# Performance work log

Measured on AMD Instinct MI355X. Metric: run time of the kernel, lower is better.

The kernel has to match this reference:

```python
import jax, jax.numpy as jnp
import numpy as np

D_MODEL = 2048
EXPAND = 2
D_INNER = EXPAND * D_MODEL          # 4096 == d_ssm
D_STATE = 128
NGROUPS = 1
HEADDIM = 64
NHEADS = D_INNER // HEADDIM          # 64
D_CONV = 4
CHUNK = 128
D_XBC = D_INNER + 2 * NGROUPS * D_STATE   # 4352
D_IN_PROJ = 2 * D_INNER + 2 * NGROUPS * D_STATE + NHEADS  # 8512
EPS = 1e-5


def setup_inputs() -> dict:
    key = jax.random.key(0)
    ks = jax.random.split(key, 9)
    u = jax.random.normal(ks[0], (2, 2048, D_MODEL), dtype=jnp.float32)
    W_in = jax.random.normal(ks[1], (D_IN_PROJ, D_MODEL), dtype=jnp.float32) / np.sqrt(D_MODEL)
    conv_w = jax.random.normal(ks[2], (D_XBC, D_CONV), dtype=jnp.float32) / np.sqrt(D_CONV)
    conv_b = jax.random.normal(ks[3], (D_XBC,), dtype=jnp.float32) * 0.1
    dt_bias = jnp.log(jnp.expm1(jax.random.uniform(ks[4], (NHEADS,), minval=0.001, maxval=0.1)))
    A_log = jnp.log(jax.random.uniform(ks[5], (NHEADS,), minval=1.0, maxval=16.0))
    D = jnp.ones((NHEADS,), dtype=jnp.float32)
    norm_weight = jnp.ones((D_INNER,), dtype=jnp.float32)
    W_out = jax.random.normal(ks[8], (D_MODEL, D_INNER), dtype=jnp.float32) / np.sqrt(D_INNER)
    return {"u": u, "W_in": W_in, "conv_w": conv_w, "conv_b": conv_b,
            "dt_bias": dt_bias, "A_log": A_log, "D": D,
            "norm_weight": norm_weight, "W_out": W_out}


def _causal_conv1d(xBC, conv_w, conv_b):
    # xBC: [b, l, d]; depthwise causal conv of width D_CONV, then SiLU
    x = jnp.transpose(xBC, (0, 2, 1))                      # [b, d, l]
    x = jnp.pad(x, ((0, 0), (0, 0), (D_CONV - 1, 0)))
    y = jax.lax.conv_general_dilated(
        x, conv_w[:, None, :], window_strides=(1,), padding='VALID',
        feature_group_count=D_XBC, dimension_numbers=('NCH', 'OIH', 'NCH'))
    y = y + conv_b[None, :, None]
    return jnp.transpose(jax.nn.silu(y), (0, 2, 1))        # [b, l, d]


def _ssd(x, dt, A, B, C, D):
    # x: [b,l,h,p]; dt: [b,l,h] (post-softplus); A: [h]; B,C: [b,l,g,n]; D: [h]
    b, L, h, p = x.shape
    n = B.shape[-1]
    c = L // CHUNK
    hpg = h // NGROUPS
    Bh = jnp.repeat(B, hpg, axis=2)                        # [b,l,h,n]
    Ch = jnp.repeat(C, hpg, axis=2)
    xr = x.reshape(b, c, CHUNK, h, p)
    dtr = dt.reshape(b, c, CHUNK, h)
    Br = Bh.reshape(b, c, CHUNK, h, n)
    Cr = Ch.reshape(b, c, CHUNK, h, n)
    xdt = xr * dtr[..., None]                              # [b,c,l,h,p]
    dA = jnp.transpose((dt * A[None, None, :]).reshape(b, c, CHUNK, h), (0, 3, 1, 2))  # [b,h,c,l]
    A_cs = jnp.cumsum(dA, axis=-1)                         # [b,h,c,l]
    # intra-chunk decay matrix L[i,j] = exp(sum_{j+1..i} dA), lower-triangular
    diff = A_cs[..., :, None] - A_cs[..., None, :]         # [b,h,c,l,s]
    mask = jnp.tril(jnp.ones((CHUNK, CHUNK), dtype=bool))
    Lmat = jnp.where(mask, jnp.exp(jnp.where(mask, diff, 0.0)), 0.0)
    Y_diag = jnp.einsum('bclhn,bcshn,bhcls,bcshp->bclhp', Cr, Br, Lmat, xdt)
    decay_states = jnp.exp(A_cs[..., -1:] - A_cs)          # [b,h,c,l]
    states = jnp.einsum('bclhn,bhcl,bclhp->bchpn', Br, decay_states, xdt)
    chunk_decay = jnp.exp(A_cs[..., -1])                   # [b,h,c]
    # inter-chunk recurrence over c chunks
    def step(carry, inp):
        s, d = inp                                         # s:[b,h,p,n], d:[b,h]
        return carry * d[..., None, None] + s, carry
    init = jnp.zeros((b, h, p, n), dtype=x.dtype)
    _, prev = jax.lax.scan(step, init,
                           (jnp.transpose(states, (1, 0, 2, 3, 4)),
                            jnp.transpose(chunk_decay, (2, 0, 1))))
    prev_states = jnp.transpose(prev, (1, 0, 2, 3, 4))     # [b,c,h,p,n]
    Y_off = jnp.einsum('bclhn,bchpn,bhcl->bclhp', Cr, prev_states, jnp.exp(A_cs))
    Y = (Y_diag + Y_off).reshape(b, L, h, p) + x * D[None, None, :, None]
    return Y


def reference(u, W_in, conv_w, conv_b, dt_bias, A_log, D, norm_weight, W_out):
    b, L, _ = u.shape
    zxbcdt = jnp.einsum('bld,ed->ble', u, W_in)            # [b,l,8512]
    z = zxbcdt[..., :D_INNER]
    xBC = zxbcdt[..., D_INNER:D_INNER + D_XBC]
    dt = zxbcdt[..., D_INNER + D_XBC:]                     # [b,l,h]
    xBC = _causal_conv1d(xBC, conv_w, conv_b)
    x = xBC[..., :D_INNER]
    B = xBC[..., D_INNER:D_INNER + NGROUPS * D_STATE].reshape(b, L, NGROUPS, D_STATE)
    C = xBC[..., D_INNER + NGROUPS * D_STATE:].reshape(b, L, NGROUPS, D_STATE)
    dt = jax.nn.softplus(dt + dt_bias[None, None, :])
    A = -jnp.exp(A_log)
    y = _ssd(x.reshape(b, L, NHEADS, HEADDIM), dt, A, B, C, D)
    y = y.reshape(b, L, D_INNER)
    # gated RMSNorm (norm_before_gate=False): norm(y * silu(z))
    yg = y * jax.nn.silu(z)
    y = yg * jax.lax.rsqrt(jnp.mean(yg * yg, axis=-1, keepdims=True) + EPS) * norm_weight
    return jnp.einsum('bld,ed->ble', y, W_out)
```

## Files before the change

### kernel.cpp

```cpp
#include <hip/hip_runtime.h>
#include <cstdint>
#include <cstddef>

#define SEQ     2048
#define NBATCH  2
#define BL      (NBATCH*SEQ)
#define DMODEL  2048
#define DINNER  4096
#define DSTATE  128
#define HEADDIM 64
#define NHEADS  64
#define DXBC    4352
#define DPROJ   8512
#define NPAD    8704
#define NCHUNK  16
#define CHUNKL  128

typedef __bf16 bf16x8_t __attribute__((ext_vector_type(8)));
typedef float f32x4_t __attribute__((ext_vector_type(4)));
typedef unsigned short u16x8_t __attribute__((ext_vector_type(8)));
typedef unsigned short u16x4_t __attribute__((ext_vector_type(4)));
typedef __attribute__((address_space(1))) unsigned int as1_u32;
typedef __attribute__((address_space(3))) unsigned int as3_u32;

__device__ __forceinline__ unsigned short f2bf(float f) {
  unsigned u = __builtin_bit_cast(unsigned, f);
  u += 0x7FFFu + ((u >> 16) & 1u);
  return (unsigned short)(u >> 16);
}
__device__ __forceinline__ float bf2f(unsigned short h) {
  unsigned u = ((unsigned)h) << 16;
  return __builtin_bit_cast(float, u);
}
__device__ __forceinline__ void gload16(const void* g, void* l) {
  __builtin_amdgcn_global_load_lds((const as1_u32*)g, (as3_u32*)l, 16, 0, 0);
}
__device__ __forceinline__ f32x4_t mfma16(u16x8_t a, u16x8_t b, f32x4_t c) {
  return __builtin_amdgcn_mfma_f32_16x16x32_bf16(
      __builtin_bit_cast(bf16x8_t, a), __builtin_bit_cast(bf16x8_t, b), c, 0, 0, 0);
}
__device__ __forceinline__ float siluf(float x) { return x / (1.f + __expf(-x)); }

__global__ __launch_bounds__(256) void cvt_kernel(const float* __restrict__ src,
                                                  unsigned short* __restrict__ dst, int n) {
  int idx = (blockIdx.x * 256 + threadIdx.x) * 4;
  if (idx >= n) return;
  float4 v = *(const float4*)&src[idx];
  u16x4_t o; o[0] = f2bf(v.x); o[1] = f2bf(v.y); o[2] = f2bf(v.z); o[3] = f2bf(v.w);
  *(u16x4_t*)&dst[idx] = o;
}

__global__ __launch_bounds__(256) void cvt_win_kernel(const float* __restrict__ W,
                                                      unsigned short* __restrict__ dst) {
  int idx = (blockIdx.x * 256 + threadIdx.x) * 4;
  if (idx >= NPAD * DMODEL) return;
  int e = idx / DMODEL;
  u16x4_t o;
  if (e < DPROJ) {
    float4 v = *(const float4*)&W[idx];
    o[0] = f2bf(v.x); o[1] = f2bf(v.y); o[2] = f2bf(v.z); o[3] = f2bf(v.w);
  } else {
    o[0] = 0; o[1] = 0; o[2] = 0; o[3] = 0;
  }
  *(u16x4_t*)&dst[idx] = o;
}

template <int WM, bool BF16OUT>
__global__ __launch_bounds__(512, 2) void gemm256_kernel(const unsigned short* __restrict__ A,
                                                         const unsigned short* __restrict__ B,
                                                         void* __restrict__ Cp,
                                                         int M, int N, int K, int gx) {
  constexpr int BM  = 32 * WM;
  constexpr int AUB = BM * 64;
  constexpr int BUB = 16384;
  constexpr int BUF = AUB + BUB;
  constexpr int LA  = AUB / 8192;
  constexpr int LB  = 2;
  __shared__ __attribute__((aligned(16))) char lds[4 * BUF];

  const int nwg = gridDim.x;
  const int q8 = nwg >> 3;
  const int lid = blockIdx.x;
  const int newid = (lid & 7) * q8 + (lid >> 3);
  const int band = newid / (gx * 4);
  const int idx  = newid % (gx * 4);
  const int n0 = (idx >> 2) * 256;
  const int m0 = (band * 4 + (idx & 3)) * BM;

  const int t = threadIdx.x, lane = t & 63, w = t >> 6;
  const int wm = w >> 2, wn = w & 3;
  const int NK = K >> 5;
  const int kslot = (lane >> 4) * 16;

  f32x4_t acc[WM][4];
#pragma unroll
  for (int i = 0; i < WM; ++i)
#pragma unroll
    for (int j = 0; j < 4; ++j) acc[i][j] = (f32x4_t){0.f, 0.f, 0.f, 0.f};

  auto stage_unit = [&](int u) {
    if (u >= 2 * NK) return;
    const int Tt = u >> 1;
    char* base = lds + (Tt & 3) * BUF + ((u & 1) ? AUB : 0);
    const unsigned short* G = (u & 1) ? B : A;
    const int g0 = (u & 1) ? n0 : m0;
    const int k0 = Tt << 5;
    if (u & 1) {
#pragma unroll
      for (int i = 0; i < LB; ++i) {
        int o = i * 8192 + t * 16;
        int row = o >> 6;
        int cb = (o & 63) ^ (((row >> 1) & 3) << 4);
        gload16(&G[(size_t)(g0 + row) * K + k0 + (cb >> 1)], base + o);
      }
    } else {
#pragma unroll
      for (int i = 0; i < LA; ++i) {
        int o = i * 8192 + t * 16;
        int row = o >> 6;
        int cb = (o & 63) ^ (((row >> 1) & 3) << 4);
        gload16(&G[(size_t)(g0 + row) * K + k0 + (cb >> 1)], base + o);
      }
    }
  };
  auto rdA = [&](int bq, int mr) -> u16x8_t {
    int row = wm * (BM / 2) + mr * 16 + (lane & 15);
    int byte = bq * BUF + row * 64 + (kslot ^ (((row >> 1) & 3) << 4));
    return *(const u16x8_t*)(lds + byte);
  };
  auto rdB = [&](int bq, int nr) -> u16x8_t {
    int row = wn * 64 + nr * 16 + (lane & 15);
    int byte = bq * BUF + AUB + row * 64 + (kslot ^ (((row >> 1) & 3) << 4));
    return *(const u16x8_t*)(lds + byte);
  };

#pragma unroll
  for (int u = 0; u < 6; ++u) stage_unit(u);
  if constexpr (WM == 8) asm volatile("s_waitcnt vmcnt(8)" ::: "memory");
  else                   asm volatile("s_waitcnt vmcnt(6)" ::: "memory");
  asm volatile("" ::: "memory");
  __builtin_amdgcn_s_barrier();

  for (int T = 0; T < NK; ++T) {
    const int bq = T & 3;
    u16x8_t af[WM], bfr[4];
#pragma unroll
    for (int mr = 0; mr < WM; ++mr) af[mr] = rdA(bq, mr);
    bfr[0] = rdB(bq, 0);
    bfr[1] = rdB(bq, 1);
    stage_unit(2 * T + 6);
    asm volatile("" ::: "memory");
    __builtin_amdgcn_s_barrier();
    asm volatile("s_waitcnt lgkmcnt(0)" ::: "memory");
    __builtin_amdgcn_sched_barrier(0);
    __builtin_amdgcn_s_setprio(1);
#pragma unroll
    for (int mr = 0; mr < WM; ++mr) {
      acc[mr][0] = mfma16(af[mr], bfr[0], acc[mr][0]);
      acc[mr][1] = mfma16(af[mr], bfr[1], acc[mr][1]);
    }
    __builtin_amdgcn_s_setprio(0);
    asm volatile("" ::: "memory");
    __builtin_amdgcn_s_barrier();
    bfr[2] = rdB(bq, 2);
    bfr[3] = rdB(bq, 3);
    stage_unit(2 * T + 7);
    asm volatile("s_waitcnt lgkmcnt(0)" ::: "memory");
    __builtin_amdgcn_sched_barrier(0);
    __builtin_amdgcn_s_setprio(1);
#pragma unroll
    for (int mr = 0; mr < WM; ++mr) {
      acc[mr][2] = mfma16(af[mr], bfr[2], acc[mr][2]);
      acc[mr][3] = mfma16(af[mr], bfr[3], acc[mr][3]);
    }
    __builtin_amdgcn_s_setprio(0);
    if (T < NK - 3) {
      if constexpr (WM == 8) asm volatile("s_waitcnt vmcnt(8)" ::: "memory");
      else                   asm volatile("s_waitcnt vmcnt(6)" ::: "memory");
    } else if (T == NK - 3) {
      if constexpr (WM == 8) asm volatile("s_waitcnt vmcnt(4)" ::: "memory");
      else                   asm volatile("s_waitcnt vmcnt(3)" ::: "memory");
    } else if (T == NK - 2) {
      asm volatile("s_waitcnt vmcnt(0)" ::: "memory");
    }
    asm volatile("" ::: "memory");
    __builtin_amdgcn_s_barrier();
  }

#pragma unroll
  for (int mr = 0; mr < WM; ++mr) {
    const int mbase = m0 + wm * (BM / 2) + mr * 16 + (lane >> 4) * 4;
#pragma unroll
    for (int nr = 0; nr < 4; ++nr) {
      const int n = n0 + wn * 64 + nr * 16 + (lane & 15);
#pragma unroll
      for (int r = 0; r < 4; ++r) {
        if (BF16OUT) ((unsigned short*)Cp)[(size_t)(mbase + r) * N + n] = f2bf(acc[mr][nr][r]);
        else         ((float*)Cp)[(size_t)(mbase + r) * N + n] = acc[mr][nr][r];
      }
    }
  }
}

__global__ __launch_bounds__(256) void conv_kernel(const unsigned short* __restrict__ zx,
                                                   const float* __restrict__ conv_w,
                                                   const float* __restrict__ conv_b,
                                                   unsigned short* __restrict__ xc) {
  long long idx = (long long)blockIdx.x * 256 + threadIdx.x;
  if (idx >= (long long)BL * DXBC) return;
  int e = (int)(idx % DXBC);
  int bl = (int)(idx / DXBC);
  int l = bl % SEQ, b = bl / SEQ;
  float acc = conv_b[e];
#pragma unroll
  for (int wi = 0; wi < 4; ++wi) {
    int ll = l - 3 + wi;
    if (ll >= 0) acc += bf2f(zx[((size_t)b * SEQ + ll) * NPAD + DINNER + e]) * conv_w[e * 4 + wi];
  }
  xc[(size_t)bl * DXBC + e] = f2bf(siluf(acc));
}

__global__ __launch_bounds__(128) void dt_kernel(const unsigned short* __restrict__ zx,
                                                 const float* __restrict__ dt_bias,
                                                 const float* __restrict__ A_log,
                                                 float* __restrict__ dt_soft,
                                                 float* __restrict__ Acs,
                                                 float* __restrict__ cdecay) {
  int blk = blockIdx.x;
  int c = blk & 15, h = (blk >> 4) & 63, b = blk >> 10;
  int i = threadIdx.x;
  int l = c * CHUNKL + i;
  float raw = bf2f(zx[((size_t)b * SEQ + l) * NPAD + (DINNER + DXBC) + h]) + dt_bias[h];
  float dt = (raw > 20.f) ? raw : log1pf(__expf(raw));
  dt_soft[((size_t)b * 64 + h) * SEQ + l] = dt;
  float A = -__expf(A_log[h]);
  __shared__ float sbuf[128];
  sbuf[i] = dt * A;
  __syncthreads();
  for (int ofs = 1; ofs < 128; ofs <<= 1) {
    float v = (i >= ofs) ? sbuf[i - ofs] : 0.f;
    __syncthreads();
    sbuf[i] += v;
    __syncthreads();
  }
  float cs = sbuf[i];
  Acs[(((size_t)b * 64 + h) * 16 + c) * 128 + i] = cs;
  if (i == 127) cdecay[((size_t)b * 64 + h) * 16 + c] = __expf(cs);
}

__global__ __launch_bounds__(256) void xdt_kernel(const unsigned short* __restrict__ xc,
                                                  const float* __restrict__ dt_soft,
                                                  unsigned short* __restrict__ xdtT) {
  int blk = blockIdx.x;
  int lt = blk & 15, h = (blk >> 4) & 63, b = blk >> 10;
  __shared__ unsigned short tile[128][66];
  __shared__ float dts[128];
  int t = threadIdx.x;
  const unsigned short* xg = xc + ((size_t)b * SEQ + lt * 128) * DXBC + h * 64;
#pragma unroll
  for (int k = 0; k < 32; ++k) {
    int idx = t + k * 256;
    int row = idx >> 6, col = idx & 63;
    tile[row][col] = xg[(size_t)row * DXBC + col];
  }
  if (t < 128) dts[t] = dt_soft[((size_t)b * 64 + h) * SEQ + lt * 128 + t];
  __syncthreads();
  unsigned short* xo = xdtT + (((size_t)b * 64 + h) * 64) * SEQ + lt * 128;
#pragma unroll
  for (int k = 0; k < 32; ++k) {
    int idx = t + k * 256;
    int p = idx >> 7, j = idx & 127;
    xo[(size_t)p * SEQ + j] = f2bf(bf2f(tile[j][p]) * dts[j]);
  }
}

__global__ __launch_bounds__(256) void btr_kernel(const unsigned short* __restrict__ xc,
                                                  unsigned short* __restrict__ BT) {
  int blk = blockIdx.x;
  int lt = blk & 15, b = blk >> 4;
  __shared__ unsigned short tile[128][129];
  int t = threadIdx.x;
  const unsigned short* src = xc + ((size_t)b * SEQ + lt * 128) * DXBC + DINNER;
#pragma unroll
  for (int k = 0; k < 64; ++k) {
    int idx = t + k * 256;
    int j = idx >> 7, n = idx & 127;
    tile[j][n] = src[(size_t)j * DXBC + n];
  }
  __syncthreads();
  unsigned short* dst = BT + (size_t)b * 128 * SEQ + lt * 128;
#pragma unroll
  for (int k = 0; k < 64; ++k) {
    int idx = t + k * 256;
    int n = idx >> 7, j = idx & 127;
    dst[(size_t)n * SEQ + j] = tile[j][n];
  }
}

__global__ __launch_bounds__(256) void ssd_states_kernel(const unsigned short* __restrict__ BT,
                                                         const unsigned short* __restrict__ xdtT,
                                                         const float* __restrict__ Acs,
                                                         float* __restrict__ states) {
  int blk = blockIdx.x;
  int h = blk & 63, c = (blk >> 6) & 15, b = blk >> 10;
  __shared__ unsigned short BTs[128 * 128];
  __shared__ unsigned short xs[64 * 128];
  __shared__ float dec[128];
  int t = threadIdx.x, lane = t & 63, w = t >> 6, wr = w >> 1, wc = w & 1;
  int srow = t >> 4, scol = (t & 15) * 8;
  const unsigned short* BTb = BT + (size_t)b * 128 * SEQ + c * 128;
#pragma unroll
  for (int s = 0; s < 8; ++s) {
    int r = s * 16 + srow;
    gload16(&BTb[(size_t)r * SEQ + scol], &BTs[r * 128 + scol]);
  }
  const unsigned short* xb = xdtT + (((size_t)b * 64 + h) * 64) * SEQ + c * 128;
#pragma unroll
  for (int s = 0; s < 4; ++s) {
    int r = s * 16 + srow;
    gload16(&xb[(size_t)r * SEQ + scol], &xs[r * 128 + scol]);
  }
  const float* acsr = Acs + (((size_t)b * 64 + h) * 16 + c) * 128;
  float alast = acsr[127];
  if (t < 128) dec[t] = __expf(alast - acsr[t]);
  __syncthreads();

  f32x4_t acc[2][4];
#pragma unroll
  for (int i = 0; i < 2; ++i)
#pragma unroll
    for (int j = 0; j < 4; ++j) acc[i][j] = (f32x4_t){0.f, 0.f, 0.f, 0.f};
#pragma unroll
  for (int ks = 0; ks < 4; ++ks) {
    const int kk = ks * 32 + (lane >> 4) * 8;
    float d8[8];
#pragma unroll
    for (int e = 0; e < 8; ++e) d8[e] = dec[kk + e];
    u16x8_t af[2], bfr[4];
#pragma unroll
    for (int i = 0; i < 2; ++i) {
      u16x8_t raw = *(const u16x8_t*)&xs[(wr * 32 + i * 16 + (lane & 15)) * 128 + kk];
      u16x8_t sc;
#pragma unroll
      for (int e = 0; e < 8; ++e) sc[e] = f2bf(bf2f(raw[e]) * d8[e]);
      af[i] = sc;
    }
#pragma unroll
    for (int j = 0; j < 4; ++j)
      bfr[j] = *(const u16x8_t*)&BTs[(wc * 64 + j * 16 + (lane & 15)) * 128 + kk];
#pragma unroll
    for (int i = 0; i < 2; ++i)
#pragma unroll
      for (int j = 0; j < 4; ++j) acc[i][j] = mfma16(af[i], bfr[j], acc[i][j]);
  }
  float* so = states + ((((size_t)b * 16 + c) * 64 + h) * 64) * 128;
#pragma unroll
  for (int i = 0; i < 2; ++i) {
    int pbase = wr * 32 + i * 16 + (lane >> 4) * 4;
#pragma unroll
    for (int j = 0; j < 4; ++j) {
      int n = wc * 64 + j * 16 + (lane & 15);
#pragma unroll
      for (int r = 0; r < 4; ++r) so[(size_t)(pbase + r) * 128 + n] = acc[i][j][r];
    }
  }
}

__global__ __launch_bounds__(256) void ssd_scan_kernel(const float* __restrict__ states,
                                                       const float* __restrict__ cdecay,
                                                       unsigned short* __restrict__ prevb) {
  int blk = blockIdx.x;
  int s = blk & 7, h = (blk >> 3) & 63, b = blk >> 9;
  int t = threadIdx.x;
  float carry[4] = {0.f, 0.f, 0.f, 0.f};
  const float* cd = cdecay + ((size_t)b * 64 + h) * 16;
  for (int c = 0; c < 16; ++c) {
    const float* sp = states + (((size_t)(b * 16 + c) * 64 + h) * 64) * 128;
    unsigned short* pp = prevb + (((size_t)(b * 16 + c) * 64 + h) * 64) * 128;
    float d = cd[c];
#pragma unroll
    for (int k = 0; k < 4; ++k) {
      int e = s * 1024 + k * 256 + t;
      pp[e] = f2bf(carry[k]);
      carry[k] = carry[k] * d + sp[e];
    }
  }
}

__global__ __launch_bounds__(256) void ssd_y_kernel(const unsigned short* __restrict__ xc,
                                                    const unsigned short* __restrict__ xdtT,
                                                    const unsigned short* __restrict__ prevb,
                                                    const float* __restrict__ Acs,
                                                    const float* __restrict__ Dp,
                                                    unsigned short* __restrict__ Y) {
  int blk = blockIdx.x;
  int h = blk & 63, c = (blk >> 6) & 15, b = blk >> 10;
  __shared__ unsigned short Bs[128 * 128];
  __shared__ unsigned short Cs[128 * 128];
  __shared__ unsigned short xs[64 * 128];
  __shared__ unsigned short ps[64 * 128];
  __shared__ float acs_s[128];
  int t = threadIdx.x, lane = t & 63, w = t >> 6, wr = w >> 1, wc = w & 1;
  int srow = t >> 4, scol = (t & 15) * 8;
  const unsigned short* Bg = xc + ((size_t)b * SEQ + c * 128) * DXBC + DINNER;
  const unsigned short* Cg = Bg + DSTATE;
#pragma unroll
  for (int s = 0; s < 8; ++s) {
    int r = s * 16 + srow;
    gload16(&Bg[(size_t)r * DXBC + scol], &Bs[r * 128 + scol]);
    gload16(&Cg[(size_t)r * DXBC + scol], &Cs[r * 128 + scol]);
  }
  const unsigned short* xg = xdtT + (((size_t)b * 64 + h) * 64) * SEQ + c * 128;
#pragma unroll
  for (int s = 0; s < 4; ++s) {
    int r = s * 16 + srow;
    gload16(&xg[(size_t)r * SEQ + scol], &xs[r * 128 + scol]);
  }
  const unsigned short* pg = prevb + ((((size_t)b * 16 + c) * 64 + h) * 64) * 128;
#pragma unroll
  for (int s = 0; s < 4; ++s) {
    int r = s * 16 + srow;
    gload16(&pg[r * 128 + scol], &ps[r * 128 + scol]);
  }
  const float* acsr = Acs + (((size_t)b * 64 + h) * 16 + c) * 128;
  if (t < 128) acs_s[t] = acsr[t];
  __syncthreads();

  f32x4_t cbt[4][4];
#pragma unroll
  for (int i = 0; i < 4; ++i)
#pragma unroll
    for (int j = 0; j < 4; ++j) cbt[i][j] = (f32x4_t){0.f, 0.f, 0.f, 0.f};
#pragma unroll
  for (int ks = 0; ks < 4; ++ks) {
    const int kk = ks * 32 + (lane >> 4) * 8;
    u16x8_t af[4], bfr[4];
#pragma unroll
    for (int i = 0; i < 4; ++i) {
      af[i]  = *(const u16x8_t*)&Bs[(wr * 64 + i * 16 + (lane & 15)) * 128 + kk];
      bfr[i] = *(const u16x8_t*)&Cs[(wc * 64 + i * 16 + (lane & 15)) * 128 + kk];
    }
#pragma unroll
    for (int i = 0; i < 4; ++i)
#pragma unroll
      for (int j = 0; j < 4; ++j) cbt[i][j] = mfma16(af[i], bfr[j], cbt[i][j]);
  }
  __syncthreads();
#pragma unroll
  for (int fi = 0; fi < 4; ++fi) {
#pragma unroll
    for (int fj = 0; fj < 4; ++fj) {
      int i = wc * 64 + fj * 16 + (lane & 15);
      int jb = wr * 64 + fi * 16 + (lane >> 4) * 4;
      float ai = acs_s[i];
      u16x4_t m4;
#pragma unroll
      for (int r = 0; r < 4; ++r) {
        int j = jb + r;
        float v = (i >= j) ? cbt[fi][fj][r] * __expf(ai - acs_s[j]) : 0.f;
        m4[r] = f2bf(v);
      }
      *(u16x4_t*)&Bs[i * 128 + jb] = m4;
    }
  }
  __syncthreads();

  f32x4_t accY[4][2], accO[4][2];
#pragma unroll
  for (int i = 0; i < 4; ++i)
#pragma unroll
    for (int j = 0; j < 2; ++j) {
      accY[i][j] = (f32x4_t){0.f, 0.f, 0.f, 0.f};
      accO[i][j] = (f32x4_t){0.f, 0.f, 0.f, 0.f};
    }
#pragma unroll
  for (int ks = 0; ks < 4; ++ks) {
    const int kk = ks * 32 + (lane >> 4) * 8;
    u16x8_t af[4], bfr[2], cf[4], pf[2];
#pragma unroll
    for (int i = 0; i < 4; ++i) {
      af[i] = *(const u16x8_t*)&Bs[(wr * 64 + i * 16 + (lane & 15)) * 128 + kk];
      cf[i] = *(const u16x8_t*)&Cs[(wr * 64 + i * 16 + (lane & 15)) * 128 + kk];
    }
#pragma unroll
    for (int j = 0; j < 2; ++j) {
      bfr[j] = *(const u16x8_t*)&xs[(wc * 32 + j * 16 + (lane & 15)) * 128 + kk];
      pf[j]  = *(const u16x8_t*)&ps[(wc * 32 + j * 16 + (lane & 15)) * 128 + kk];
    }
#pragma unroll
    for (int i = 0; i < 4; ++i)
#pragma unroll
      for (int j = 0; j < 2; ++j) {
        accY[i][j] = mfma16(af[i], bfr[j], accY[i][j]);
        accO[i][j] = mfma16(cf[i], pf[j], accO[i][j]);
      }
  }
  float Dh = Dp[h];
  unsigned short* Yo = Y + ((size_t)b * SEQ + c * 128) * DINNER + h * 64;
  const unsigned short* xo = xc + ((size_t)b * SEQ + c * 128) * DXBC + h * 64;
#pragma unroll
  for (int fi = 0; fi < 4; ++fi) {
    int ibase = wr * 64 + fi * 16 + (lane >> 4) * 4;
#pragma unroll
    for (int r = 0; r < 4; ++r) {
      int i = ibase + r;
      float esc = __expf(acs_s[i]);
#pragma unroll
      for (int fj = 0; fj < 2; ++fj) {
        int p = wc * 32 + fj * 16 + (lane & 15);
        float v = accY[fi][fj][r] + accO[fi][fj][r] * esc + bf2f(xo[(size_t)i * DXBC + p]) * Dh;
        Yo[(size_t)i * DINNER + p] = f2bf(v);
      }
    }
  }
}

__global__ __launch_bounds__(256) void norm_kernel(const unsigned short* __restrict__ Y,
                                                   const unsigned short* __restrict__ zx,
                                                   const float* __restrict__ nw,
                                                   unsigned short* __restrict__ yn) {
  int bl = blockIdx.x;
  const unsigned short* yr = Y + (size_t)bl * DINNER;
  const unsigned short* zr = zx + (size_t)bl * NPAD;
  int t = threadIdx.x;
  float vals[16];
  float ss = 0.f;
#pragma unroll
  for (int k = 0; k < 16; ++k) {
    int d = t + k * 256;
    float g = bf2f(yr[d]) * siluf(bf2f(zr[d]));
    vals[k] = g;
    ss += g * g;
  }
#pragma unroll
  for (int o = 32; o > 0; o >>= 1) ss += __shfl_down(ss, o, 64);
  __shared__ float red[4];
  if ((t & 63) == 0) red[t >> 6] = ss;
  __syncthreads();
  float tot = red[0] + red[1] + red[2] + red[3];
  float rs = rsqrtf(tot * (1.f / (float)DINNER) + 1e-5f);
#pragma unroll
  for (int k = 0; k < 16; ++k) {
    int d = t + k * 256;
    yn[(size_t)bl * DINNER + d] = f2bf(vals[k] * rs * nw[d]);
  }
}

extern "C" void kernel_launch(void* const* d_in, const int* in_sizes, int n_in,
                              void* d_out, int out_size, void* d_ws, size_t ws_size,
                              hipStream_t stream) {
  const float* u       = (const float*)d_in[0];
  const float* W_in    = (const float*)d_in[1];
  const float* conv_w  = (const float*)d_in[2];
  const float* conv_b  = (const float*)d_in[3];
  const float* dt_bias = (const float*)d_in[4];
  const float* A_log   = (const float*)d_in[5];
  const float* Dv      = (const float*)d_in[6];
  const float* norm_w  = (const float*)d_in[7];
  const float* W_out   = (const float*)d_in[8];
  float* out = (float*)d_out;
  (void)in_sizes; (void)n_in; (void)out_size;

  const size_t SZ_UBF    = (size_t)BL * DMODEL * 2;
  const size_t SZ_WIN    = (size_t)NPAD * DMODEL * 2;
  const size_t SZ_XDTT   = (size_t)NBATCH * NHEADS * HEADDIM * SEQ * 2;
  const size_t SZ_ZX     = (size_t)BL * NPAD * 2;
  const size_t SZ_XC     = (size_t)BL * DXBC * 2;
  const size_t SZ_BT     = (size_t)NBATCH * DSTATE * SEQ * 2;
  const size_t SZ_DTS    = (size_t)NBATCH * NHEADS * SEQ * 4;
  const size_t SZ_ACS    = (size_t)NBATCH * NHEADS * NCHUNK * 128 * 4;
  const size_t SZ_CDEC   = (size_t)NBATCH * NHEADS * NCHUNK * 4;
  const size_t SZ_STATES = (size_t)NBATCH * NCHUNK * NHEADS * HEADDIM * DSTATE * 4;
  const size_t SZ_PREV   = (size_t)NBATCH * NCHUNK * NHEADS * HEADDIM * DSTATE * 2;
  const size_t REGION_A  = SZ_UBF + SZ_WIN;

  char* ws = (char*)d_ws;
  size_t off = 0;
  auto alloc = [&](size_t bytes) { char* p = ws + off; off += (bytes + 255) & ~(size_t)255; return p; };

  char* regionA = alloc(REGION_A);
  unsigned short* zx     = (unsigned short*)alloc(SZ_ZX);
  unsigned short* xc     = (unsigned short*)alloc(SZ_XC);
  unsigned short* BT     = (unsigned short*)alloc(SZ_BT);
  float* dt_soft         = (float*)alloc(SZ_DTS);
  float* Acs             = (float*)alloc(SZ_ACS);
  float* cdecay          = (float*)alloc(SZ_CDEC);
  char* statesYb         = alloc(SZ_STATES);
  char* prevYn           = alloc(SZ_PREV);
  if (off > ws_size) return;

  unsigned short* u_bf    = (unsigned short*)regionA;
  unsigned short* win_bf  = (unsigned short*)(regionA + SZ_UBF);
  unsigned short* xdtT    = (unsigned short*)regionA;
  unsigned short* wout_bf = (unsigned short*)(regionA + SZ_XDTT);
  float* states           = (float*)statesYb;
  unsigned short* Yb      = (unsigned short*)statesYb;
  unsigned short* prevb   = (unsigned short*)prevYn;
  unsigned short* yn      = (unsigned short*)prevYn;

  cvt_kernel<<<dim3((BL * DMODEL / 4 + 255) / 256), dim3(256), 0, stream>>>(u, u_bf, BL * DMODEL);
  cvt_win_kernel<<<dim3(NPAD * DMODEL / 4 / 256), dim3(256), 0, stream>>>(W_in, win_bf);

  gemm256_kernel<8, true><<<dim3((NPAD / 256) * (BL / 256)), dim3(512), 0, stream>>>(
      u_bf, win_bf, zx, BL, NPAD, DMODEL, NPAD / 256);

  cvt_kernel<<<dim3((DMODEL * DINNER / 4 + 255) / 256), dim3(256), 0, stream>>>(W_out, wout_bf, DMODEL * DINNER);

  conv_kernel<<<dim3((int)(((size_t)BL * DXBC + 255) / 256)), dim3(256), 0, stream>>>(zx, conv_w, conv_b, xc);

  dt_kernel<<<dim3(NBATCH * NHEADS * NCHUNK), dim3(128), 0, stream>>>(zx, dt_bias, A_log, dt_soft, Acs, cdecay);

  xdt_kernel<<<dim3(NBATCH * NHEADS * NCHUNK), dim3(256), 0, stream>>>(xc, dt_soft, xdtT);
  btr_kernel<<<dim3(NBATCH * (SEQ / 128)), dim3(256), 0, stream>>>(xc, BT);

  ssd_states_kernel<<<dim3(NBATCH * NCHUNK * NHEADS), dim3(256), 0, stream>>>(BT, xdtT, Acs, states);
  ssd_scan_kernel<<<dim3(NBATCH * NHEADS * 8), dim3(256), 0, stream>>>(states, cdecay, prevb);
  ssd_y_kernel<<<dim3(NBATCH * NCHUNK * NHEADS), dim3(256), 0, stream>>>(xc, xdtT, prevb, Acs, Dv, Yb);

  norm_kernel<<<dim3(BL), dim3(256), 0, stream>>>(Yb, zx, norm_w, yn);

  gemm256_kernel<4, false><<<dim3((DMODEL / 256) * (BL / 128)), dim3(512), 0, stream>>>(
      yn, wout_bf, out, BL, DMODEL, DINNER, DMODEL / 256);
}
```

Measured before the change: 568.5 us.

## Switch GEMM to double-buffered LDS pipeline and vectorize conv kernel

The GEMM kernel drops from a 4-deep LDS ring with split half-tile MFMA phases to a 2-stage double buffer. Each K step waits on global loads, reads all fragments, issues the next tile's loads and then runs all MFMAs. This halves LDS use, which could raise occupancy, but leaves less prefetch depth to hide global latency. Separately, the depthwise conv kernel now processes 8 channels per thread with 16-byte vector loads and stores instead of one scalar element per thread.

```diff
diff --git a/kernel.cpp b/kernel.cpp
--- a/kernel.cpp
+++ b/kernel.cpp
@@ -76,7 +76,8 @@
   constexpr int BUF = AUB + BUB;
   constexpr int LA  = AUB / 8192;
   constexpr int LB  = 2;
-  __shared__ __attribute__((aligned(16))) char lds[4 * BUF];
+  constexpr int LT  = LA + LB;
+  __shared__ __attribute__((aligned(16))) char lds[2 * BUF];
 
   const int nwg = gridDim.x;
   const int q8 = nwg >> 3;
@@ -101,7 +102,7 @@
   auto stage_unit = [&](int u) {
     if (u >= 2 * NK) return;
     const int Tt = u >> 1;
-    char* base = lds + (Tt & 3) * BUF + ((u & 1) ? AUB : 0);
+    char* base = lds + (Tt & 1) * BUF + ((u & 1) ? AUB : 0);
     const unsigned short* G = (u & 1) ? B : A;
     const int g0 = (u & 1) ? n0 : m0;
     const int k0 = Tt << 5;
@@ -135,56 +136,34 @@
   };
 
 #pragma unroll
-  for (int u = 0; u < 6; ++u) stage_unit(u);
-  if constexpr (WM == 8) asm volatile("s_waitcnt vmcnt(8)" ::: "memory");
-  else                   asm volatile("s_waitcnt vmcnt(6)" ::: "memory");
-  asm volatile("" ::: "memory");
-  __builtin_amdgcn_s_barrier();
+  for (int u = 0; u < 4; ++u) stage_unit(u);
 
   for (int T = 0; T < NK; ++T) {
-    const int bq = T & 3;
+    const int bq = T & 1;
+    if (T < NK - 1) {
+      if constexpr (LT == 4) asm volatile("s_waitcnt vmcnt(4)" ::: "memory");
+      else                   asm volatile("s_waitcnt vmcnt(3)" ::: "memory");
+    } else {
+      asm volatile("s_waitcnt vmcnt(0)" ::: "memory");
+    }
+    __builtin_amdgcn_s_barrier();
+    asm volatile("" ::: "memory");
     u16x8_t af[WM], bfr[4];
 #pragma unroll
     for (int mr = 0; mr < WM; ++mr) af[mr] = rdA(bq, mr);
-    bfr[0] = rdB(bq, 0);
-    bfr[1] = rdB(bq, 1);
-    stage_unit(2 * T + 6);
+#pragma unroll
+    for (int nr = 0; nr < 4; ++nr) bfr[nr] = rdB(bq, nr);
+    asm volatile("s_waitcnt lgkmcnt(0)" ::: "memory");
+    __builtin_amdgcn_s_barrier();
     asm volatile("" ::: "memory");
-    __builtin_amdgcn_s_barrier();
-    asm volatile("s_waitcnt lgkmcnt(0)" ::: "memory");
-    __builtin_amdgcn_sched_barrier(0);
+    stage_unit(2 * T + 4);
+    stage_unit(2 * T + 5);
     __builtin_amdgcn_s_setprio(1);
 #pragma unroll
-    for (int mr = 0; mr < WM; ++mr) {
-      acc[mr][0] = mfma16(af[mr], bfr[0], acc[mr][0]);
-      acc[mr][1] = mfma16(af[mr], bfr[1], acc[mr][1]);
-    }
+    for (int mr = 0; mr < WM; ++mr)
+#pragma unroll
+      for (int nr = 0; nr < 4; ++nr) acc[mr][nr] = mfma16(af[mr], bfr[nr], acc[mr][nr]);
     __builtin_amdgcn_s_setprio(0);
-    asm volatile("" ::: "memory");
-    __builtin_amdgcn_s_barrier();
-    bfr[2] = rdB(bq, 2);
-    bfr[3] = rdB(bq, 3);
-    stage_unit(2 * T + 7);
-    asm volatile("s_waitcnt lgkmcnt(0)" ::: "memory");
-    __builtin_amdgcn_sched_barrier(0);
-    __builtin_amdgcn_s_setprio(1);
-#pragma unroll
-    for (int mr = 0; mr < WM; ++mr) {
-      acc[mr][2] = mfma16(af[mr], bfr[2], acc[mr][2]);
-      acc[mr][3] = mfma16(af[mr], bfr[3], acc[mr][3]);
-    }
-    __builtin_amdgcn_s_setprio(0);
-    if (T < NK - 3) {
-      if constexpr (WM == 8) asm volatile("s_waitcnt vmcnt(8)" ::: "memory");
-      else                   asm volatile("s_waitcnt vmcnt(6)" ::: "memory");
-    } else if (T == NK - 3) {
-      if constexpr (WM == 8) asm volatile("s_waitcnt vmcnt(4)" ::: "memory");
-      else                   asm volatile("s_waitcnt vmcnt(3)" ::: "memory");
-    } else if (T == NK - 2) {
-      asm volatile("s_waitcnt vmcnt(0)" ::: "memory");
-    }
-    asm volatile("" ::: "memory");
-    __builtin_amdgcn_s_barrier();
   }
 
 #pragma unroll
@@ -206,18 +185,28 @@
                                                    const float* __restrict__ conv_w,
                                                    const float* __restrict__ conv_b,
                                                    unsigned short* __restrict__ xc) {
-  long long idx = (long long)blockIdx.x * 256 + threadIdx.x;
-  if (idx >= (long long)BL * DXBC) return;
-  int e = (int)(idx % DXBC);
-  int bl = (int)(idx / DXBC);
+  int idx = blockIdx.x * 256 + threadIdx.x;
+  if (idx >= BL * (DXBC / 8)) return;
+  int e8 = (idx % (DXBC / 8)) * 8;
+  int bl = idx / (DXBC / 8);
   int l = bl % SEQ, b = bl / SEQ;
-  float acc = conv_b[e];
+  float acc[8];
+#pragma unroll
+  for (int j = 0; j < 8; ++j) acc[j] = conv_b[e8 + j];
+  const unsigned short* zrow = zx + (size_t)b * SEQ * NPAD + DINNER + e8;
 #pragma unroll
   for (int wi = 0; wi < 4; ++wi) {
     int ll = l - 3 + wi;
-    if (ll >= 0) acc += bf2f(zx[((size_t)b * SEQ + ll) * NPAD + DINNER + e]) * conv_w[e * 4 + wi];
-  }
-  xc[(size_t)bl * DXBC + e] = f2bf(siluf(acc));
+    if (ll >= 0) {
+      u16x8_t v = *(const u16x8_t*)(zrow + (size_t)ll * NPAD);
+#pragma unroll
+      for (int j = 0; j < 8; ++j) acc[j] += bf2f(v[j]) * conv_w[(e8 + j) * 4 + wi];
+    }
+  }
+  u16x8_t o;
+#pragma unroll
+  for (int j = 0; j < 8; ++j) o[j] = f2bf(siluf(acc[j]));
+  *(u16x8_t*)(xc + (size_t)bl * DXBC + e8) = o;
 }
 
 __global__ __launch_bounds__(128) void dt_kernel(const unsigned short* __restrict__ zx,
@@ -606,7 +595,7 @@
 
   cvt_kernel<<<dim3((DMODEL * DINNER / 4 + 255) / 256), dim3(256), 0, stream>>>(W_out, wout_bf, DMODEL * DINNER);
 
-  conv_kernel<<<dim3((int)(((size_t)BL * DXBC + 255) / 256)), dim3(256), 0, stream>>>(zx, conv_w, conv_b, xc);
+  conv_kernel<<<dim3(BL * (DXBC / 8) / 256), dim3(256), 0, stream>>>(zx, conv_w, conv_b, xc);
 
   dt_kernel<<<dim3(NBATCH * NHEADS * NCHUNK), dim3(128), 0, stream>>>(zx, dt_bias, A_log, dt_soft, Acs, cdecay);
 
```

Result: slower. 623.0 us (+9.6%).
